# Kernel optimization log

Measured on AMD Instinct MI355X. Metric: run time of the kernel, lower is better.

Reference implementation:

```python
import jax, jax.numpy as jnp
import numpy as np
from jax import lax

B, C, H, W = 64, 512, 20, 15
N = H * W  # must be 300 (ChannelAttention dim)
EPS = 1e-5


def layernorm(x, w, b):
    m = x.mean(-1, keepdims=True)
    v = x.var(-1, keepdims=True)
    return (x - m) * lax.rsqrt(v + EPS) * w + b


def batchnorm(x, w, b):  # training-mode BN over (B,H,W), x: (B,C,H,W)
    m = x.mean((0, 2, 3), keepdims=True)
    v = x.var((0, 2, 3), keepdims=True)
    return (x - m) * lax.rsqrt(v + EPS) * w[None, :, None, None] + b[None, :, None, None]


def cross_linear_attn(x1, x2, kv1_w, kv2_w, heads):
    # x: (B, n, c); kv_w: (2c, c). Linear-attention variant: softmax over channel axis of k^T v.
    b, n, c = x1.shape
    d = c // heads
    scale = d ** -0.5

    def split_q(x):
        return x.reshape(b, n, heads, d).transpose(0, 2, 1, 3)  # (b,h,n,d)

    def kv(x, w):
        t = (x @ w.T).reshape(b, n, 2, heads, d).transpose(2, 0, 3, 1, 4)
        return t[0], t[1]  # each (b,h,n,d)

    q1, q2 = split_q(x1), split_q(x2)
    k1, v1 = kv(x1, kv1_w)
    k2, v2 = kv(x2, kv2_w)

    def ctx(k, v):  # (b,h,d,d), softmax over dim -2
        return jax.nn.softmax(jnp.einsum('bhnd,bhne->bhde', k, v) * scale, axis=-2)

    c1, c2 = ctx(k1, v1), ctx(k2, v2)

    def out(q, cx):
        return jnp.einsum('bhnd,bhde->bhne', q, cx).transpose(0, 2, 1, 3).reshape(b, n, c)

    return out(q1, c2), out(q2, c1)  # cross: q1 uses ctx2, q2 uses ctx1


def conv1x1(x, w):  # x: (B,Ci,H,W), w: (Co,Ci)
    return jnp.einsum('oi,bihw->bohw', w, x)


def setup_inputs() -> dict:
    key = jax.random.key(0)
    ks = jax.random.split(key, 24)
    g = lambda i, shape, s=0.02: jax.random.normal(ks[i], shape, jnp.float32) * s
    inp = {
        'x1': jax.random.normal(ks[0], (B, C, H, W), jnp.float32),
        'x2': jax.random.normal(ks[1], (B, C, H, W), jnp.float32),
        # CrossPath channel_proj1/2: Linear(C, 2C) + LayerNorm(2C)
        'cp1_w': g(2, (2 * C, C)), 'cp1_b': jnp.zeros((2 * C,), jnp.float32),
        'ln1_w': jnp.ones((2 * C,), jnp.float32), 'ln1_b': jnp.zeros((2 * C,), jnp.float32),
        'cp2_w': g(3, (2 * C, C)), 'cp2_b': jnp.zeros((2 * C,), jnp.float32),
        'ln2_w': jnp.ones((2 * C,), jnp.float32), 'ln2_b': jnp.zeros((2 * C,), jnp.float32),
        # SpatialAttention (dim=C, heads=8) kv linears, no bias
        's_kv1_w': g(4, (2 * C, C)), 's_kv2_w': g(5, (2 * C, C)),
        # ChannelAttention (dim=N=300, heads=4) kv linears, no bias
        'c_kv1_w': g(6, (2 * N, N)), 'c_kv2_w': g(7, (2 * N, N)),
        # ChannelEmbed(2C -> C)
        'res_w': g(8, (C, 2 * C), np.sqrt(2.0 / C)),
        'ce1_w': g(9, (C, 2 * C), np.sqrt(2.0 / C)), 'ce1_b': jnp.zeros((C,), jnp.float32),
        'dw_w': g(10, (C, 1, 3, 3), np.sqrt(2.0 / 9.0)), 'dw_b': jnp.zeros((C,), jnp.float32),
        'ce3_w': g(11, (C, C), np.sqrt(2.0 / C)), 'ce3_b': jnp.zeros((C,), jnp.float32),
        'bn_e_w': jnp.ones((C,), jnp.float32), 'bn_e_b': jnp.zeros((C,), jnp.float32),
        'bn_o_w': jnp.ones((C,), jnp.float32), 'bn_o_b': jnp.zeros((C,), jnp.float32),
    }
    return inp


def reference(x1, x2, cp1_w, cp1_b, ln1_w, ln1_b, cp2_w, cp2_b, ln2_w, ln2_b,
              s_kv1_w, s_kv2_w, c_kv1_w, c_kv2_w,
              res_w, ce1_w, ce1_b, dw_w, dw_b, ce3_w, ce3_b,
              bn_e_w, bn_e_b, bn_o_w, bn_o_b):
    b, c, h, w = x1.shape
    n = h * w
    t1 = x1.reshape(b, c, n).transpose(0, 2, 1)  # (B,N,C)
    t2 = x2.reshape(b, c, n).transpose(0, 2, 1)

    a1 = jax.nn.relu(layernorm(t1 @ cp1_w.T + cp1_b, ln1_w, ln1_b))
    a2 = jax.nn.relu(layernorm(t2 @ cp2_w.T + cp2_b, ln2_w, ln2_b))
    c1, s1 = a1[..., :c], a1[..., c:]
    c2, s2 = a2[..., :c], a2[..., c:]

    v1, v2 = cross_linear_attn(s1, s2, s_kv1_w, s_kv2_w, heads=8)
    z1, z2 = cross_linear_attn(c1.transpose(0, 2, 1), c2.transpose(0, 2, 1),
                               c_kv1_w, c_kv2_w, heads=4)
    s = v1 + v2                                  # (B,N,C)
    cc = (z1 + z2).transpose(0, 2, 1)            # (B,N,C)

    merge = jnp.concatenate([s, cc], axis=-1)    # (B,N,2C)
    xm = merge.transpose(0, 2, 1).reshape(b, 2 * c, h, w)

    residual = conv1x1(xm, res_w)
    e = conv1x1(xm, ce1_w) + ce1_b[None, :, None, None]
    e = lax.conv_general_dilated(e, dw_w, (1, 1), 'SAME',
                                 dimension_numbers=('NCHW', 'OIHW', 'NCHW'),
                                 feature_group_count=c) + dw_b[None, :, None, None]
    e = jnp.where(e >= 0, e, 0.01 * e)  # LeakyReLU(0.01)
    e = conv1x1(e, ce3_w) + ce3_b[None, :, None, None]
    e = batchnorm(e, bn_e_w, bn_e_b)
    return batchnorm(residual + e, bn_o_w, bn_o_b)
```

## Files before the change

### kernel.cpp

```cpp
#include <hip/hip_runtime.h>

typedef unsigned short u16;
typedef __attribute__((ext_vector_type(8))) short bh8;
typedef __attribute__((ext_vector_type(4))) float f4;

__device__ __forceinline__ u16 f2b(float f){
  unsigned int u = __float_as_uint(f);
  u += 0x7fffu + ((u >> 16) & 1u);
  return (u16)(u >> 16);
}
__device__ __forceinline__ float b2f(u16 h){
  return __uint_as_float(((unsigned int)h) << 16);
}
__device__ __forceinline__ void gl16(const u16* g, u16* l){
  __builtin_amdgcn_global_load_lds((const __attribute__((address_space(1))) void*)g,
                                   (__attribute__((address_space(3))) void*)l, 16, 0, 0);
}

__global__ void pack_plain(const float* __restrict__ src, u16* __restrict__ dst, int count){
  int i = blockIdx.x*256 + threadIdx.x;
  if (i < count) dst[i] = f2b(src[i]);
}
__global__ void pack_ckv_k(const float* __restrict__ src, u16* __restrict__ dst){
  int i = blockIdx.x*256 + threadIdx.x;
  int nn = i / 320, kk = i - (i/320)*320;
  int t_ = (nn >= 320) ? 1 : 0;
  int rem = nn - t_*320;
  int hh = rem / 80, dd = rem - hh*80;
  int kh = kk / 80, kd = kk - kh*80;
  float v = 0.f;
  if (dd < 75 && kd < 75)
    v = src[(size_t)(t_*300 + hh*75 + dd)*300 + (kh*75 + kd)];
  dst[i] = f2b(v);
}
__global__ void pack_dw(const float* __restrict__ src, u16* __restrict__ dst){
  int i = blockIdx.x*256 + threadIdx.x;
  if (i < 4608){
    int t = i >> 9, c = i & 511;
    dst[i] = f2b(src[c*9 + t]);
  }
}
__global__ void pad_zero(u16* __restrict__ slack){
  const int j = blockIdx.x*256 + threadIdx.x;
  if (j < 2048) slack[j] = 0;
}

__global__ __launch_bounds__(256)
void transpose_k(const float* __restrict__ x, u16* __restrict__ t)
{
  __shared__ float tile[32][33];
  const int n0 = blockIdx.x * 32, c0 = blockIdx.y * 32, b = blockIdx.z;
  const int ln = threadIdx.x & 31, lr = threadIdx.x >> 5;
  #pragma unroll
  for (int q = 0; q < 4; q++) {
    const int c = c0 + lr + q*8, n = n0 + ln;
    tile[lr + q*8][ln] = (n < 300) ? x[((long)b*512 + c)*300 + n] : 0.f;
  }
  __syncthreads();
  #pragma unroll
  for (int q = 0; q < 4; q++) {
    const int n = n0 + lr + q*8;
    if (n < 300) t[((long)b*300 + n)*512 + c0 + ln] = f2b(tile[ln][lr + q*8]);
  }
}

template<int OUTF, int HASB>
__global__ __launch_bounds__(512, 2)
void gemm256(const u16* __restrict__ A, int lda,
             const u16* __restrict__ Bw, const u16* __restrict__ Bw2, int ldb, long mhalf,
             u16* __restrict__ Cb, float* __restrict__ Cf, int ldc,
             const float* __restrict__ bias, const float* __restrict__ bias2, int K)
{
  __shared__ u16 As[2][16384];
  __shared__ u16 Bs[2][16384];
  const int tid = threadIdx.x;
  const int gx = gridDim.x;
  const int nwg = gx * gridDim.y;
  const int flat = blockIdx.y * gx + blockIdx.x;
  const int qq = nwg >> 3, rr = nwg & 7, xcd = flat & 7, lin = flat >> 3;
  const int newid = (xcd < rr ? xcd*(qq+1) : rr*(qq+1) + (xcd-rr)*qq) + lin;
  const long n0 = (long)(newid % gx) * 256;
  const long m0 = (long)(newid / gx) * 256;
  const u16* Bwp = Bw; const float* bp = bias;
  if (Bw2 != nullptr && m0 >= mhalf){ Bwp = Bw2; bp = bias2; }
  const int wave = tid >> 6, lane = tid & 63;
  const int l15 = lane & 15, lg = lane >> 4;
  const int wr = (wave >> 2) * 128;
  const int wc = (wave & 3) * 64;
  const int srow = tid >> 3;
  const int gseg = ((tid & 7) ^ (srow & 7)) * 8;
  const u16* Ag[4]; const u16* Bg[4];
  #pragma unroll
  for (int q = 0; q < 4; q++){
    Ag[q] = A   + (m0 + q*64 + srow) * (long)lda + gseg;
    Bg[q] = Bwp + (n0 + q*64 + srow) * (long)ldb + gseg;
  }
  int roA[8], roB[4];
  #pragma unroll
  for (int i = 0; i < 8; i++){ const int rA = wr + i*16 + l15; roA[i] = rA*64 + ((lg ^ (rA & 7)) * 8); }
  #pragma unroll
  for (int i = 0; i < 4; i++){ const int rB = wc + i*16 + l15; roB[i] = rB*64 + ((lg ^ (rB & 7)) * 8); }
  f4 acc[8][4] = {};
  const int NT = K >> 6;
  #pragma unroll
  for (int q = 0; q < 4; q++){
    gl16(Ag[q], &As[0][(q*512 + tid)*8]);
    gl16(Bg[q], &Bs[0][(q*512 + tid)*8]);
  }
  asm volatile("s_waitcnt vmcnt(0)" ::: "memory");
  __builtin_amdgcn_sched_barrier(0);
  __builtin_amdgcn_s_barrier();
  __builtin_amdgcn_sched_barrier(0);
  int cur = 0;
  for (int t = 0; t < NT; t++) {
    if (t + 1 < NT) {
      const int kt = (t + 1) << 6;
      const int nb = cur ^ 1;
      #pragma unroll
      for (int q = 0; q < 4; q++){
        gl16(Ag[q] + kt, &As[nb][(q*512 + tid)*8]);
        gl16(Bg[q] + kt, &Bs[nb][(q*512 + tid)*8]);
      }
    }
    #pragma unroll
    for (int ks = 0; ks < 2; ks++){
      const int kx = ks * 32;
      bh8 af[8], bf[4];
      #pragma unroll
      for (int mi = 0; mi < 8; mi++) af[mi] = *(const bh8*)&As[cur][roA[mi] ^ kx];
      #pragma unroll
      for (int ni = 0; ni < 4; ni++) bf[ni] = *(const bh8*)&Bs[cur][roB[ni] ^ kx];
      __builtin_amdgcn_s_setprio(1);
      #pragma unroll
      for (int mi = 0; mi < 8; mi++)
        #pragma unroll
        for (int ni = 0; ni < 4; ni++)
          acc[mi][ni] = __builtin_amdgcn_mfma_f32_16x16x32_bf16(af[mi], bf[ni], acc[mi][ni], 0, 0, 0);
      __builtin_amdgcn_s_setprio(0);
    }
    if (t + 1 < NT) {
      asm volatile("s_waitcnt vmcnt(0)" ::: "memory");
      __builtin_amdgcn_sched_barrier(0);
      __builtin_amdgcn_s_barrier();
      __builtin_amdgcn_sched_barrier(0);
      cur ^= 1;
    }
  }
  if (OUTF == 2) {
    u16* resb16 = (u16*)Cf;
    if (n0 < 512) {
      #pragma unroll
      for (int ni = 0; ni < 4; ni++) {
        const long cn = n0 + wc + ni*16 + l15;
        #pragma unroll
        for (int mi = 0; mi < 8; mi++)
          #pragma unroll
          for (int r = 0; r < 4; r++) {
            const long cm = m0 + wr + mi*16 + lg*4 + r;
            resb16[cm * ldc + cn] = f2b(acc[mi][ni][r]);
          }
      }
    } else {
      #pragma unroll
      for (int ni = 0; ni < 4; ni++) {
        const long cn = n0 - 512 + wc + ni*16 + l15;
        const float bv = bias[cn];
        #pragma unroll
        for (int mi = 0; mi < 8; mi++)
          #pragma unroll
          for (int r = 0; r < 4; r++) {
            const long cm = m0 + wr + mi*16 + lg*4 + r;
            Cb[cm * ldc + cn] = f2b(acc[mi][ni][r] + bv);
          }
      }
    }
  } else {
    #pragma unroll
    for (int ni = 0; ni < 4; ni++) {
      const long cn = n0 + wc + ni*16 + l15;
      const float bv = HASB ? bp[cn] : 0.0f;
      #pragma unroll
      for (int mi = 0; mi < 8; mi++)
        #pragma unroll
        for (int r = 0; r < 4; r++) {
          const long cm = m0 + wr + mi*16 + lg*4 + r;
          Cb[cm * ldc + cn] = f2b(acc[mi][ni][r] + bv);
        }
    }
  }
}

template<int OUTF, int HASB>
__global__ __launch_bounds__(512)
void gemm_k(const u16* __restrict__ A, int lda,
            const u16* __restrict__ Bw, const u16* __restrict__ Bw2, int ldb, long mhalf,
            u16* __restrict__ Cb, float* __restrict__ Cf, int ldc,
            const float* __restrict__ bias, const float* __restrict__ bias2, int K)
{
  __shared__ u16 As[3][8192];
  __shared__ u16 Bs[3][4096];
  const int tid = threadIdx.x;
  const int gx = gridDim.x;
  const int nwg = gx * gridDim.y;
  const int flat = blockIdx.y * gx + blockIdx.x;
  const int qq = nwg >> 3, rr = nwg & 7, xcd = flat & 7, lin = flat >> 3;
  const int newid = (xcd < rr ? xcd*(qq+1) : rr*(qq+1) + (xcd-rr)*qq) + lin;
  const long n0 = (long)(newid % gx) * 128;
  const long m0 = (long)(newid / gx) * 256;
  const u16* Bwp = Bw; const float* bp = bias;
  if (Bw2 != nullptr && m0 >= mhalf){ Bwp = Bw2; bp = bias2; }
  const int wave = tid >> 6, lane = tid & 63;
  const int l15 = lane & 15, lg = lane >> 4;
  const int wr = (wave >> 1) * 64, wc = (wave & 1) * 64;
  const int arow = tid >> 2;
  const int aseg = ((tid & 3) ^ ((arow >> 1) & 3)) * 8;
  const u16* Ag0 = A + (m0 + arow) * (long)lda + aseg;
  const u16* Ag1 = A + (m0 + 128 + arow) * (long)lda + aseg;
  const u16* Bg0 = Bwp + (n0 + arow) * (long)ldb + aseg;
  const int to8 = tid * 8;
  int roA[4], roB[4];
  #pragma unroll
  for (int i = 0; i < 4; i++){
    const int rA = wr + i*16 + l15;
    roA[i] = rA*32 + ((lg ^ ((rA >> 1) & 3)) * 8);
    const int rB = wc + i*16 + l15;
    roB[i] = rB*32 + ((lg ^ ((rB >> 1) & 3)) * 8);
  }
  f4 acc[4][4] = {};
  const int NT = K >> 5;
  {
    gl16(Ag0, &As[0][to8]); gl16(Ag1, &As[0][4096 + to8]); gl16(Bg0, &Bs[0][to8]);
    gl16(Ag0 + 32, &As[1][to8]); gl16(Ag1 + 32, &As[1][4096 + to8]); gl16(Bg0 + 32, &Bs[1][to8]);
  }
  int rd = 0;
  for (int t = 0; t < NT; t++) {
    if (t < NT - 1) { asm volatile("s_waitcnt vmcnt(3)" ::: "memory"); }
    else            { asm volatile("s_waitcnt vmcnt(0)" ::: "memory"); }
    __builtin_amdgcn_sched_barrier(0);
    __builtin_amdgcn_s_barrier();
    __builtin_amdgcn_sched_barrier(0);
    if (t + 2 < NT) {
      int wb = rd + 2; if (wb >= 3) wb -= 3;
      const int kt = (t + 2) << 5;
      gl16(Ag0 + kt, &As[wb][to8]); gl16(Ag1 + kt, &As[wb][4096 + to8]); gl16(Bg0 + kt, &Bs[wb][to8]);
    }
    bh8 af[4], bf[4];
    #pragma unroll
    for (int mi = 0; mi < 4; mi++) af[mi] = *(const bh8*)&As[rd][roA[mi]];
    #pragma unroll
    for (int ni = 0; ni < 4; ni++) bf[ni] = *(const bh8*)&Bs[rd][roB[ni]];
    #pragma unroll
    for (int mi = 0; mi < 4; mi++)
      #pragma unroll
      for (int ni = 0; ni < 4; ni++)
        acc[mi][ni] = __builtin_amdgcn_mfma_f32_16x16x32_bf16(af[mi], bf[ni], acc[mi][ni], 0, 0, 0);
    rd++; if (rd == 3) rd = 0;
  }
  #pragma unroll
  for (int ni = 0; ni < 4; ni++) {
    const long cn = n0 + wc + ni*16 + l15;
    const float bv = HASB ? bp[cn] : 0.0f;
    #pragma unroll
    for (int mi = 0; mi < 4; mi++) {
      #pragma unroll
      for (int r = 0; r < 4; r++) {
        const long cm = m0 + wr + mi*16 + lg*4 + r;
        const float v = acc[mi][ni][r] + bv;
        if (OUTF) Cf[cm * ldc + cn] = v;
        else      Cb[cm * ldc + cn] = f2b(v);
      }
    }
  }
}

__global__ __launch_bounds__(256)
void ln_kernel(const u16* __restrict__ apre, const float* __restrict__ lw, const float* __restrict__ lb,
               u16* __restrict__ s, u16* __restrict__ cT)
{
  __shared__ u16 tile[40][520];
  const int bh = blockIdx.x;
  const int b = bh >> 2, h = bh & 3;
  const int z = blockIdx.y;
  const int dd0 = z ? 40 : 0;
  const int ndd = z ? 35 : 40;
  const int segbase = z ? 5 : 0;
  const int tid = threadIdx.x, w = tid >> 6, lane = tid & 63;
  const int r0 = b*300 + h*75 + dd0;
  for (int dl = w; dl < ndd; dl += 4){
    const int r = r0 + dl;
    const u16* row = apre + (size_t)r*1024 + lane*8;
    const bh8 vc = *(const bh8*)row;
    const bh8 vs = *(const bh8*)(row + 512);
    float fc[8], fs[8];
    float sm = 0.f, sq = 0.f;
    #pragma unroll
    for (int j = 0; j < 8; j++){
      fc[j] = b2f((u16)vc[j]); fs[j] = b2f((u16)vs[j]);
      sm += fc[j] + fs[j];
      sq += fc[j]*fc[j] + fs[j]*fs[j];
    }
    #pragma unroll
    for (int o = 32; o; o >>= 1){ sm += __shfl_xor(sm, o); sq += __shfl_xor(sq, o); }
    const float mean = sm * (1.f/1024.f);
    const float rstd = rsqrtf(sq*(1.f/1024.f) - mean*mean + 1e-5f);
    bh8 oc, os;
    #pragma unroll
    for (int j = 0; j < 8; j++){
      const int c = lane*8 + j;
      const float y1 = (fc[j]-mean)*rstd*lw[c] + lb[c];
      oc[j] = (short)f2b(fmaxf(y1, 0.f));
      const float y2 = (fs[j]-mean)*rstd*lw[512+c] + lb[512+c];
      os[j] = (short)f2b(fmaxf(y2, 0.f));
    }
    *(bh8*)&tile[dl][lane*8] = oc;
    *(bh8*)&s[(size_t)r*512 + lane*8] = os;
  }
  __syncthreads();
  for (int i = tid; i < 2560; i += 256){
    const int c = i / 5, sg = i - (i/5)*5;
    const int seg = segbase + sg;
    bh8 ov;
    #pragma unroll
    for (int j = 0; j < 8; j++){
      const int dl = seg*8 + j - dd0;
      ov[j] = (short)((dl >= 0 && dl < ndd) ? tile[dl][c] : (u16)0);
    }
    *(bh8*)&cT[((size_t)b*512 + c)*320 + h*80 + seg*8] = ov;
  }
}

template<int D, int DREAL, int OS>
__global__ __launch_bounds__(256)
void ctx_kernel(const u16* __restrict__ kva, const u16* __restrict__ kvb,
                u16* __restrict__ outp, int K, int RS, int VOFF, float scale)
{
  constexpr int NT = D/16, MT = D/16, MTL = (MT+3)/4, SEG = D/8;
  __shared__ u16 vT[D][40];
  __shared__ u16 kT[D][40];
  const int h = blockIdx.x, b = blockIdx.y, iq = blockIdx.z;
  const int Hn = gridDim.x;
  const u16* base = (iq ? kvb : kva) + (size_t)b*K*RS + h*D;
  u16* out = outp + (((size_t)iq*64 + b)*Hn + h)*(size_t)(D*OS);
  const int tid = threadIdx.x, w = tid >> 6, lane = tid & 63, l15 = lane & 15, lg = lane >> 4;
  f4 acc[MTL][NT] = {};
  for (int k0 = 0; k0 < K; k0 += 32) {
    __syncthreads();
    for (int sI = tid; sI < 32*SEG; sI += 256) {
      const int nn = sI / SEG, dseg = sI - (sI/SEG)*SEG;
      bh8 kk = {}, vv = {};
      const int krow = k0 + nn;
      if (krow < K) {
        const u16* p = base + (size_t)krow*RS + dseg*8;
        kk = *(const bh8*)p;
        vv = *(const bh8*)(p + VOFF);
      }
      #pragma unroll
      for (int j = 0; j < 8; j++){
        kT[dseg*8+j][nn] = (u16)kk[j];
        vT[dseg*8+j][nn] = (u16)vv[j];
      }
    }
    __syncthreads();
    #pragma unroll
    for (int ii = 0; ii < MTL; ii++){
      const int mt = w + ii*4;
      if (MT % 4 != 0 && mt >= MT) break;
      const bh8 a = *(const bh8*)&vT[mt*16 + l15][lg*8];
      #pragma unroll
      for (int nt = 0; nt < NT; nt++){
        const bh8 bb = *(const bh8*)&kT[nt*16 + l15][lg*8];
        acc[ii][nt] = __builtin_amdgcn_mfma_f32_16x16x32_bf16(a, bb, acc[ii][nt], 0, 0, 0);
      }
    }
  }
  #pragma unroll
  for (int ii = 0; ii < MTL; ii++){
    const int mt = w + ii*4;
    if (MT % 4 != 0 && mt >= MT) continue;
    #pragma unroll
    for (int r = 0; r < 4; r++){
      const int e = mt*16 + lg*4 + r;
      float xs[NT]; float mx = -1e30f;
      #pragma unroll
      for (int nt = 0; nt < NT; nt++){
        float x = acc[ii][nt][r] * scale;
        if (DREAL != D && (nt*16 + l15) >= DREAL) x = -1e30f;
        xs[nt] = x; mx = fmaxf(mx, x);
      }
      mx = fmaxf(mx, __shfl_xor(mx,1)); mx = fmaxf(mx, __shfl_xor(mx,2));
      mx = fmaxf(mx, __shfl_xor(mx,4)); mx = fmaxf(mx, __shfl_xor(mx,8));
      float smv = 0.f;
      #pragma unroll
      for (int nt = 0; nt < NT; nt++){
        const float p = (xs[nt] > -1e29f) ? __expf(xs[nt]-mx) : 0.f;
        xs[nt] = p; smv += p;
      }
      smv += __shfl_xor(smv,1); smv += __shfl_xor(smv,2);
      smv += __shfl_xor(smv,4); smv += __shfl_xor(smv,8);
      const float inv = 1.f / smv;
      #pragma unroll
      for (int nt = 0; nt < NT; nt++)
        out[(size_t)e*OS + nt*16 + l15] = f2b(xs[nt]*inv);
      if (OS > D) out[(size_t)e*OS + D + l15] = 0;
    }
  }
}

__global__ __launch_bounds__(256)
void sp_out_kernel(const u16* __restrict__ s1, const u16* __restrict__ s2,
                   const u16* __restrict__ csT, u16* __restrict__ merge)
{
  const int h = blockIdx.x, b = blockIdx.y;
  const int tid = threadIdx.x, w = tid >> 6, lane = tid & 63, l15 = lane & 15, lg = lane >> 4;
  const u16* c1 = csT + (((size_t)b)*8 + h)*4096;
  const u16* c2 = csT + (((size_t)64 + b)*8 + h)*4096;
  for (int mt = w; mt < 19; mt += 4) {
    const int m = mt*16 + l15;
    const bool mv = (m < 300);
    const u16* q1 = s1 + ((size_t)b*300 + m)*512 + h*64;
    const u16* q2 = s2 + ((size_t)b*300 + m)*512 + h*64;
    f4 acc[4] = {};
    #pragma unroll
    for (int kc = 0; kc < 2; kc++){
      bh8 a1 = {}, a2 = {};
      if (mv){ a1 = *(const bh8*)(q1 + kc*32 + lg*8); a2 = *(const bh8*)(q2 + kc*32 + lg*8); }
      #pragma unroll
      for (int nt = 0; nt < 4; nt++){
        const bh8 b2v = *(const bh8*)&c2[(size_t)(nt*16+l15)*64 + kc*32 + lg*8];
        acc[nt] = __builtin_amdgcn_mfma_f32_16x16x32_bf16(a1, b2v, acc[nt], 0, 0, 0);
        const bh8 b1v = *(const bh8*)&c1[(size_t)(nt*16+l15)*64 + kc*32 + lg*8];
        acc[nt] = __builtin_amdgcn_mfma_f32_16x16x32_bf16(a2, b1v, acc[nt], 0, 0, 0);
      }
    }
    #pragma unroll
    for (int nt = 0; nt < 4; nt++)
      #pragma unroll
      for (int r = 0; r < 4; r++){
        const int mm = mt*16 + lg*4 + r;
        if (mm < 300)
          merge[((size_t)b*300 + mm)*1024 + h*64 + nt*16 + l15] = f2b(acc[nt][r]);
      }
  }
}

__global__ __launch_bounds__(256)
void ch_out_kernel(const u16* __restrict__ cT1, const u16* __restrict__ cT2,
                   const u16* __restrict__ ccT, u16* __restrict__ merge)
{
  const int cb = blockIdx.x, h = blockIdx.y, b = blockIdx.z;
  const int tid = threadIdx.x, w = tid >> 6, lane = tid & 63, l15 = lane & 15, lg = lane >> 4;
  const int chbase = cb*128 + w*32;
  f4 acc[5][2] = {};
  #pragma unroll
  for (int oi = 0; oi < 2; oi++){
    const u16* Am = ccT + (((size_t)((oi==0)?1:0)*64 + b)*4 + h)*(size_t)(80*96);
    const u16* qb = (oi==0) ? cT1 : cT2;
    #pragma unroll
    for (int kc = 0; kc < 3; kc++){
      bh8 bf[2];
      #pragma unroll
      for (int nf = 0; nf < 2; nf++){
        const int ch = chbase + nf*16 + l15;
        bf[nf] = *(const bh8*)&qb[((size_t)b*512 + ch)*320 + h*80 + kc*32 + lg*8];
      }
      #pragma unroll
      for (int mt = 0; mt < 5; mt++){
        const bh8 a = *(const bh8*)&Am[(size_t)(mt*16+l15)*96 + kc*32 + lg*8];
        #pragma unroll
        for (int nf = 0; nf < 2; nf++)
          acc[mt][nf] = __builtin_amdgcn_mfma_f32_16x16x32_bf16(a, bf[nf], acc[mt][nf], 0, 0, 0);
      }
    }
  }
  #pragma unroll
  for (int mt = 0; mt < 5; mt++)
    #pragma unroll
    for (int nf = 0; nf < 2; nf++)
      #pragma unroll
      for (int r = 0; r < 4; r++){
        const int e = mt*16 + lg*4 + r;
        if (e < 75)
          merge[((size_t)b*300 + h*75 + e)*1024 + 512 + chbase + nf*16 + l15] = f2b(acc[mt][nf][r]);
      }
}

__global__ __launch_bounds__(256)
void dw_kernel(const u16* __restrict__ e1, const u16* __restrict__ dwt,
               const float* __restrict__ bias, u16* __restrict__ d1)
{
  const int idx = blockIdx.x*256 + threadIdx.x;
  const int cg = idx & 63;
  const int sp = (idx >> 6) % 300;
  const int b  = idx / (64*300);
  const int c0 = cg*8;
  const int hh = sp / 15, ww = sp - hh*15;
  float acc[8];
  {
    const float4 b0 = *(const float4*)&bias[c0];
    const float4 b1 = *(const float4*)&bias[c0+4];
    acc[0]=b0.x; acc[1]=b0.y; acc[2]=b0.z; acc[3]=b0.w;
    acc[4]=b1.x; acc[5]=b1.y; acc[6]=b1.z; acc[7]=b1.w;
  }
  #pragma unroll
  for (int dy = -1; dy <= 1; dy++){
    const int h2 = hh + dy; if (h2 < 0 || h2 >= 20) continue;
    #pragma unroll
    for (int dx = -1; dx <= 1; dx++){
      const int w2 = ww + dx; if (w2 < 0 || w2 >= 15) continue;
      const bh8 vv = *(const bh8*)&e1[((size_t)b*300 + h2*15 + w2)*512 + c0];
      const int t = (dy+1)*3 + (dx+1);
      const bh8 wv = *(const bh8*)&dwt[t*512 + c0];
      #pragma unroll
      for (int j = 0; j < 8; j++)
        acc[j] += b2f((u16)vv[j]) * b2f((u16)wv[j]);
    }
  }
  bh8 ov;
  #pragma unroll
  for (int j = 0; j < 8; j++){
    float y = acc[j];
    y = (y >= 0.f) ? y : 0.01f*y;
    ov[j] = (short)f2b(y);
  }
  *(bh8*)&d1[((size_t)b*300 + sp)*512 + c0] = ov;
}

__global__ __launch_bounds__(256)
void stats_k(const u16* __restrict__ e3, const u16* __restrict__ res, float* __restrict__ st){
  const int tid = threadIdx.x;
  const int c0 = tid*2;
  const size_t r0 = (size_t)blockIdx.x * 128;
  float se0=0,se1=0,qe0=0,qe1=0,sr0=0,sr1=0,qr0=0,qr1=0,x0=0,x1=0;
  for (int rr = 0; rr < 128; rr++){
    const size_t o2 = (r0+rr)*512 + c0;
    const unsigned int eu = *(const unsigned int*)&e3[o2];
    const unsigned int ru = *(const unsigned int*)&res[o2];
    const float ex = b2f((u16)(eu & 0xffff)), ey = b2f((u16)(eu >> 16));
    const float rx = b2f((u16)(ru & 0xffff)), ry = b2f((u16)(ru >> 16));
    se0 += ex; se1 += ey; qe0 += ex*ex; qe1 += ey*ey;
    sr0 += rx; sr1 += ry; qr0 += rx*rx; qr1 += ry*ry;
    x0  += ex*rx; x1 += ey*ry;
  }
  atomicAdd(&st[c0], se0);      atomicAdd(&st[c0+1], se1);
  atomicAdd(&st[512+c0], qe0);  atomicAdd(&st[512+c0+1], qe1);
  atomicAdd(&st[1024+c0], sr0); atomicAdd(&st[1024+c0+1], sr1);
  atomicAdd(&st[1536+c0], qr0); atomicAdd(&st[1536+c0+1], qr1);
  atomicAdd(&st[2048+c0], x0);  atomicAdd(&st[2048+c0+1], x1);
}
__global__ void fin_k(float* st, const float* __restrict__ we, const float* __restrict__ be,
                      const float* __restrict__ wo, const float* __restrict__ bo){
  const int c = threadIdx.x;
  const float Nf = 19200.f, iN = 1.f/19200.f;
  const float Se = st[c], Qe = st[512+c], Sr = st[1024+c], Qr = st[1536+c], X = st[2048+c];
  const float me = Se*iN;
  const float ve = Qe*iN - me*me;
  const float ae = we[c]*rsqrtf(ve + 1e-5f);
  const float bev = be[c] - me*ae;
  const float So = Sr + ae*Se + Nf*bev;
  const float Qo = Qr + ae*ae*Qe + Nf*bev*bev + 2.f*ae*X + 2.f*bev*Sr + 2.f*ae*bev*Se;
  const float mo = So*iN;
  const float vo = Qo*iN - mo*mo;
  const float ao = wo[c]*rsqrtf(vo + 1e-5f);
  const float bov = bo[c] - mo*ao;
  st[2560+c] = ae; st[3072+c] = bev; st[3584+c] = ao; st[4096+c] = bov;
}
__global__ __launch_bounds__(256)
void final_kernel(const u16* __restrict__ res, const u16* __restrict__ e3,
                  const float* __restrict__ st, float* __restrict__ outp)
{
  __shared__ float tile[64][65];
  const int spt = blockIdx.x, cht = blockIdx.y, b = blockIdx.z;
  const int tid = threadIdx.x;
  const int sp0 = spt*64, ch0 = cht*64;
  for (int idx = tid; idx < 2048; idx += 256){
    const int cl = (idx & 31)*2, sl = idx >> 5;
    const int sp = sp0 + sl;
    float v0 = 0.f, v1 = 0.f;
    if (sp < 300){
      const size_t off = ((size_t)b*300 + sp)*512 + ch0 + cl;
      const int c = ch0 + cl;
      const unsigned int eu = *(const unsigned int*)&e3[off];
      const unsigned int ru = *(const unsigned int*)&res[off];
      const float e0 = b2f((u16)(eu & 0xffff))*st[2560+c]   + st[3072+c];
      const float e1 = b2f((u16)(eu >> 16))   *st[2560+c+1] + st[3072+c+1];
      v0 = (b2f((u16)(ru & 0xffff)) + e0)*st[3584+c]   + st[4096+c];
      v1 = (b2f((u16)(ru >> 16))    + e1)*st[3584+c+1] + st[4096+c+1];
    }
    tile[sl][cl] = v0; tile[sl][cl+1] = v1;
  }
  __syncthreads();
  for (int idx = tid; idx < 4096; idx += 256){
    const int sl = idx & 63, cl = idx >> 6;
    const int sp = sp0 + sl;
    if (sp < 300)
      outp[((size_t)b*512 + ch0 + cl)*300 + sp] = tile[sl][cl];
  }
}

extern "C" void kernel_launch(void* const* d_in, const int* in_sizes, int n_in,
                              void* d_out, int out_size, void* d_ws, size_t ws_size,
                              hipStream_t stream)
{
  const float* x1    = (const float*)d_in[0];
  const float* x2    = (const float*)d_in[1];
  const float* cp1_w = (const float*)d_in[2];
  const float* cp1_b = (const float*)d_in[3];
  const float* ln1_w = (const float*)d_in[4];
  const float* ln1_b = (const float*)d_in[5];
  const float* cp2_w = (const float*)d_in[6];
  const float* cp2_b = (const float*)d_in[7];
  const float* ln2_w = (const float*)d_in[8];
  const float* ln2_b = (const float*)d_in[9];
  const float* skv1w = (const float*)d_in[10];
  const float* skv2w = (const float*)d_in[11];
  const float* ckv1w = (const float*)d_in[12];
  const float* ckv2w = (const float*)d_in[13];
  const float* resw  = (const float*)d_in[14];
  const float* ce1w  = (const float*)d_in[15];
  const float* ce1b  = (const float*)d_in[16];
  const float* dww   = (const float*)d_in[17];
  const float* dwb   = (const float*)d_in[18];
  const float* ce3w  = (const float*)d_in[19];
  const float* ce3b  = (const float*)d_in[20];
  const float* bnew  = (const float*)d_in[21];
  const float* bneb  = (const float*)d_in[22];
  const float* bnow  = (const float*)d_in[23];
  const float* bnob  = (const float*)d_in[24];
  float* out = (float*)d_out;
  char* ws = (char*)d_ws;

  const size_t SZ_T    = (size_t)19200*512*2;
  const size_t SZ_APRE = (size_t)19200*1024*2;
  const size_t SZ_CKV  = (size_t)32768*640*2;
  const size_t SZ_CT   = (size_t)64*512*320*2;
  const size_t SZ_F32  = (size_t)19200*512*4;

  size_t off = 0;
  auto AL = [&](size_t sz){ size_t r = off; off += (sz + 255) & ~(size_t)255; return r; };
  const size_t oR0 = AL(2*SZ_T);
  const size_t oR1 = AL(2*SZ_CKV);
  const size_t oR2 = AL(2*SZ_T);
  const size_t oR3 = AL(2*SZ_CT + 4096);
  const size_t oR4 = AL(SZ_F32);
  const size_t oR5 = AL((size_t)2*64*8*64*64*2);
  const size_t oR6 = AL((size_t)2*64*4*80*96*2);
  const size_t oWcp1  = AL((size_t)1024*512*2);
  const size_t oWcp2  = AL((size_t)1024*512*2);
  const size_t oWskv1 = AL((size_t)1024*512*2);
  const size_t oWskv2 = AL((size_t)1024*512*2);
  const size_t oWckv1 = AL((size_t)640*320*2);
  const size_t oWckv2 = AL((size_t)640*320*2);
  const size_t oWresce = AL((size_t)1024*1024*2);
  const size_t oWce3  = AL((size_t)512*512*2);
  const size_t oWdw   = AL((size_t)9*512*2);
  const size_t oST    = AL(20480);
  (void)ws_size; (void)in_sizes; (void)n_in; (void)out_size;

  u16* t1    = (u16*)(ws + oR0);
  u16* merge = (u16*)(ws + oR0);
  u16* apre1 = (u16*)(ws + oR1);
  u16* ckv1  = (u16*)(ws + oR1);
  u16* s1    = (u16*)(ws + oR2);
  u16* s2    = (u16*)(ws + oR2 + SZ_T);
  u16* e1    = s1;
  u16* d1    = s2;
  u16* cT1   = (u16*)(ws + oR3);
  u16* cT2   = (u16*)(ws + oR3 + SZ_CT);
  u16* slack = (u16*)(ws + oR3 + 2*SZ_CT);
  u16* e3b   = (u16*)(ws + oR3);
  u16* resb  = (u16*)(ws + oR4);
  u16* csT   = (u16*)(ws + oR5);
  u16* ccT   = (u16*)(ws + oR6);
  u16* wcp1  = (u16*)(ws + oWcp1);
  u16* wcp2  = (u16*)(ws + oWcp2);
  u16* wskv1 = (u16*)(ws + oWskv1);
  u16* wskv2 = (u16*)(ws + oWskv2);
  u16* wckv1 = (u16*)(ws + oWckv1);
  u16* wckv2 = (u16*)(ws + oWckv2);
  u16* wresce = (u16*)(ws + oWresce);
  u16* wce3  = (u16*)(ws + oWce3);
  u16* wdw   = (u16*)(ws + oWdw);
  float* st  = (float*)(ws + oST);

  u16* t2    = t1 + 19200*512;
  u16* kv1   = apre1;
  u16* ckv2  = ckv1 + (size_t)32768*640;

  hipMemsetAsync(st, 0, 10240, stream);
  pad_zero<<<8,256,0,stream>>>(slack);
  pack_plain<<<2048,256,0,stream>>>(cp1_w, wcp1, 524288);
  pack_plain<<<2048,256,0,stream>>>(cp2_w, wcp2, 524288);
  pack_plain<<<2048,256,0,stream>>>(skv1w, wskv1, 524288);
  pack_plain<<<2048,256,0,stream>>>(skv2w, wskv2, 524288);
  pack_ckv_k<<<800,256,0,stream>>>(ckv1w, wckv1);
  pack_ckv_k<<<800,256,0,stream>>>(ckv2w, wckv2);
  pack_plain<<<2048,256,0,stream>>>(resw, wresce, 524288);
  pack_plain<<<2048,256,0,stream>>>(ce1w, wresce + 524288, 524288);
  pack_plain<<<1024,256,0,stream>>>(ce3w, wce3, 262144);
  pack_dw<<<18,256,0,stream>>>(dww, wdw);

  transpose_k<<<dim3(10,16,64),256,0,stream>>>(x1, t1);
  transpose_k<<<dim3(10,16,64),256,0,stream>>>(x2, t2);

  gemm256<0,1><<<dim3(4,150),512,0,stream>>>(t1,512, wcp1,wcp2,512, 19200L,
                                             apre1,nullptr,1024, cp1_b,cp2_b, 512);

  ln_kernel<<<dim3(256,2),256,0,stream>>>(apre1, ln1_w, ln1_b, s1, cT1);
  ln_kernel<<<dim3(256,2),256,0,stream>>>(apre1 + (size_t)19200*1024, ln2_w, ln2_b, s2, cT2);

  gemm256<0,0><<<dim3(4,150),512,0,stream>>>(s1,512, wskv1,wskv2,512, 19200L,
                                             kv1,nullptr,1024, nullptr,nullptr, 512);

  ctx_kernel<64,64,64><<<dim3(8,64,2),256,0,stream>>>(kv1, kv1 + (size_t)19200*1024, csT, 300, 1024, 512, 0.125f);

  gemm_k<0,0><<<dim3(5,256),512,0,stream>>>(cT1,320, wckv1,wckv2,320, 32768L,
                                            ckv1,nullptr,640, nullptr,nullptr, 320);

  ctx_kernel<80,75,96><<<dim3(4,64,2),256,0,stream>>>(ckv1, ckv2, ccT, 512, 640, 320, 0.115470054f);

  sp_out_kernel<<<dim3(8,64),256,0,stream>>>(s1, s2, csT, merge);
  ch_out_kernel<<<dim3(4,4,64),256,0,stream>>>(cT1, cT2, ccT, merge);

  gemm256<2,0><<<dim3(4,75),512,0,stream>>>(merge,1024, wresce,nullptr,1024, (long)1<<40,
                                            e1, (float*)resb, 512, ce1b,nullptr, 1024);

  dw_kernel<<<4800,256,0,stream>>>(e1, wdw, dwb, d1);

  gemm_k<0,1><<<dim3(4,75),512,0,stream>>>(d1,512, wce3,nullptr,512, (long)1<<40,
                                           e3b,nullptr,512, ce3b,nullptr, 512);

  stats_k<<<150,256,0,stream>>>(e3b, resb, st);
  fin_k<<<1,512,0,stream>>>(st, bnew, bneb, bnow, bnob);
  final_kernel<<<dim3(5,8,64),256,0,stream>>>(resb, e3b, st, out);
}
```

Before: 558.3 us.

## Halve GEMM K-tile to 32 with two-stage prefetch and higher occupancy

```diff
diff --git a/kernel.cpp b/kernel.cpp
--- a/kernel.cpp
+++ b/kernel.cpp
@@ -65,14 +65,14 @@
 }
 
 template<int OUTF, int HASB>
-__global__ __launch_bounds__(512, 2)
-void gemm256(const u16* __restrict__ A, int lda,
-             const u16* __restrict__ Bw, const u16* __restrict__ Bw2, int ldb, long mhalf,
-             u16* __restrict__ Cb, float* __restrict__ Cf, int ldc,
-             const float* __restrict__ bias, const float* __restrict__ bias2, int K)
-{
-  __shared__ u16 As[2][16384];
-  __shared__ u16 Bs[2][16384];
+__global__ __launch_bounds__(512, 4)
+void gemm2(const u16* __restrict__ A, int lda,
+           const u16* __restrict__ Bw, const u16* __restrict__ Bw2, int ldb, long mhalf,
+           u16* __restrict__ Cb, float* __restrict__ Cf, int ldc,
+           const float* __restrict__ bias, const float* __restrict__ bias2, int K)
+{
+  __shared__ u16 As[2][8192];
+  __shared__ u16 Bs[2][8192];
   const int tid = threadIdx.x;
   const int gx = gridDim.x;
   const int nwg = gx * gridDim.y;
@@ -87,63 +87,57 @@
   const int l15 = lane & 15, lg = lane >> 4;
   const int wr = (wave >> 2) * 128;
   const int wc = (wave & 3) * 64;
-  const int srow = tid >> 3;
-  const int gseg = ((tid & 7) ^ (srow & 7)) * 8;
-  const u16* Ag[4]; const u16* Bg[4];
-  #pragma unroll
-  for (int q = 0; q < 4; q++){
-    Ag[q] = A   + (m0 + q*64 + srow) * (long)lda + gseg;
-    Bg[q] = Bwp + (n0 + q*64 + srow) * (long)ldb + gseg;
-  }
+  const int srow = tid >> 2;
+  const int gseg = ((tid & 3) ^ ((tid >> 3) & 3)) * 8;
+  const u16* Ag0 = A   + (m0 + srow)       * (long)lda + gseg;
+  const u16* Ag1 = A   + (m0 + 128 + srow) * (long)lda + gseg;
+  const u16* Bg0 = Bwp + (n0 + srow)       * (long)ldb + gseg;
+  const u16* Bg1 = Bwp + (n0 + 128 + srow) * (long)ldb + gseg;
+  const int to8 = tid * 8;
   int roA[8], roB[4];
   #pragma unroll
-  for (int i = 0; i < 8; i++){ const int rA = wr + i*16 + l15; roA[i] = rA*64 + ((lg ^ (rA & 7)) * 8); }
-  #pragma unroll
-  for (int i = 0; i < 4; i++){ const int rB = wc + i*16 + l15; roB[i] = rB*64 + ((lg ^ (rB & 7)) * 8); }
+  for (int i = 0; i < 8; i++){ const int rA = wr + i*16 + l15; roA[i] = rA*32 + ((lg ^ ((rA >> 1) & 3)) * 8); }
+  #pragma unroll
+  for (int i = 0; i < 4; i++){ const int rB = wc + i*16 + l15; roB[i] = rB*32 + ((lg ^ ((rB >> 1) & 3)) * 8); }
   f4 acc[8][4] = {};
-  const int NT = K >> 6;
-  #pragma unroll
-  for (int q = 0; q < 4; q++){
-    gl16(Ag[q], &As[0][(q*512 + tid)*8]);
-    gl16(Bg[q], &Bs[0][(q*512 + tid)*8]);
-  }
-  asm volatile("s_waitcnt vmcnt(0)" ::: "memory");
+  const int NT = K >> 5;
+  gl16(Ag0,      &As[0][to8]); gl16(Ag1,      &As[0][4096 + to8]);
+  gl16(Bg0,      &Bs[0][to8]); gl16(Bg1,      &Bs[0][4096 + to8]);
+  gl16(Ag0 + 32, &As[1][to8]); gl16(Ag1 + 32, &As[1][4096 + to8]);
+  gl16(Bg0 + 32, &Bs[1][to8]); gl16(Bg1 + 32, &Bs[1][4096 + to8]);
+  asm volatile("s_waitcnt vmcnt(4)" ::: "memory");
   __builtin_amdgcn_sched_barrier(0);
   __builtin_amdgcn_s_barrier();
   __builtin_amdgcn_sched_barrier(0);
-  int cur = 0;
   for (int t = 0; t < NT; t++) {
+    const int cur = t & 1;
+    bh8 af[8], bf[4];
+    #pragma unroll
+    for (int mi = 0; mi < 8; mi++) af[mi] = *(const bh8*)&As[cur][roA[mi]];
+    #pragma unroll
+    for (int ni = 0; ni < 4; ni++) bf[ni] = *(const bh8*)&Bs[cur][roB[ni]];
+    __builtin_amdgcn_s_setprio(1);
+    #pragma unroll
+    for (int mi = 0; mi < 8; mi++)
+      #pragma unroll
+      for (int ni = 0; ni < 4; ni++)
+        acc[mi][ni] = __builtin_amdgcn_mfma_f32_16x16x32_bf16(af[mi], bf[ni], acc[mi][ni], 0, 0, 0);
+    __builtin_amdgcn_s_setprio(0);
     if (t + 1 < NT) {
-      const int kt = (t + 1) << 6;
-      const int nb = cur ^ 1;
-      #pragma unroll
-      for (int q = 0; q < 4; q++){
-        gl16(Ag[q] + kt, &As[nb][(q*512 + tid)*8]);
-        gl16(Bg[q] + kt, &Bs[nb][(q*512 + tid)*8]);
-      }
-    }
-    #pragma unroll
-    for (int ks = 0; ks < 2; ks++){
-      const int kx = ks * 32;
-      bh8 af[8], bf[4];
-      #pragma unroll
-      for (int mi = 0; mi < 8; mi++) af[mi] = *(const bh8*)&As[cur][roA[mi] ^ kx];
-      #pragma unroll
-      for (int ni = 0; ni < 4; ni++) bf[ni] = *(const bh8*)&Bs[cur][roB[ni] ^ kx];
-      __builtin_amdgcn_s_setprio(1);
-      #pragma unroll
-      for (int mi = 0; mi < 8; mi++)
-        #pragma unroll
-        for (int ni = 0; ni < 4; ni++)
-          acc[mi][ni] = __builtin_amdgcn_mfma_f32_16x16x32_bf16(af[mi], bf[ni], acc[mi][ni], 0, 0, 0);
-      __builtin_amdgcn_s_setprio(0);
-    }
-    if (t + 1 < NT) {
-      asm volatile("s_waitcnt vmcnt(0)" ::: "memory");
       __builtin_amdgcn_sched_barrier(0);
       __builtin_amdgcn_s_barrier();
       __builtin_amdgcn_sched_barrier(0);
-      cur ^= 1;
+      if (t + 2 < NT) {
+        const int kt = (t + 2) << 5;
+        gl16(Ag0 + kt, &As[cur][to8]); gl16(Ag1 + kt, &As[cur][4096 + to8]);
+        gl16(Bg0 + kt, &Bs[cur][to8]); gl16(Bg1 + kt, &Bs[cur][4096 + to8]);
+        asm volatile("s_waitcnt vmcnt(4)" ::: "memory");
+      } else {
+        asm volatile("s_waitcnt vmcnt(0)" ::: "memory");
+      }
+      __builtin_amdgcn_sched_barrier(0);
+      __builtin_amdgcn_s_barrier();
+      __builtin_amdgcn_sched_barrier(0);
     }
   }
   if (OUTF == 2) {
@@ -702,14 +696,14 @@
   transpose_k<<<dim3(10,16,64),256,0,stream>>>(x1, t1);
   transpose_k<<<dim3(10,16,64),256,0,stream>>>(x2, t2);
 
-  gemm256<0,1><<<dim3(4,150),512,0,stream>>>(t1,512, wcp1,wcp2,512, 19200L,
-                                             apre1,nullptr,1024, cp1_b,cp2_b, 512);
+  gemm2<0,1><<<dim3(4,150),512,0,stream>>>(t1,512, wcp1,wcp2,512, 19200L,
+                                           apre1,nullptr,1024, cp1_b,cp2_b, 512);
 
   ln_kernel<<<dim3(256,2),256,0,stream>>>(apre1, ln1_w, ln1_b, s1, cT1);
   ln_kernel<<<dim3(256,2),256,0,stream>>>(apre1 + (size_t)19200*1024, ln2_w, ln2_b, s2, cT2);
 
-  gemm256<0,0><<<dim3(4,150),512,0,stream>>>(s1,512, wskv1,wskv2,512, 19200L,
-                                             kv1,nullptr,1024, nullptr,nullptr, 512);
+  gemm2<0,0><<<dim3(4,150),512,0,stream>>>(s1,512, wskv1,wskv2,512, 19200L,
+                                           kv1,nullptr,1024, nullptr,nullptr, 512);
 
   ctx_kernel<64,64,64><<<dim3(8,64,2),256,0,stream>>>(kv1, kv1 + (size_t)19200*1024, csT, 300, 1024, 512, 0.125f);
 
@@ -721,13 +715,13 @@
   sp_out_kernel<<<dim3(8,64),256,0,stream>>>(s1, s2, csT, merge);
   ch_out_kernel<<<dim3(4,4,64),256,0,stream>>>(cT1, cT2, ccT, merge);
 
-  gemm256<2,0><<<dim3(4,75),512,0,stream>>>(merge,1024, wresce,nullptr,1024, (long)1<<40,
-                                            e1, (float*)resb, 512, ce1b,nullptr, 1024);
+  gemm2<2,0><<<dim3(4,75),512,0,stream>>>(merge,1024, wresce,nullptr,1024, (long)1<<40,
+                                          e1, (float*)resb, 512, ce1b,nullptr, 1024);
 
   dw_kernel<<<4800,256,0,stream>>>(e1, wdw, dwb, d1);
 
-  gemm_k<0,1><<<dim3(4,75),512,0,stream>>>(d1,512, wce3,nullptr,512, (long)1<<40,
-                                           e3b,nullptr,512, ce3b,nullptr, 512);
+  gemm2<0,1><<<dim3(2,75),512,0,stream>>>(d1,512, wce3,nullptr,512, (long)1<<40,
+                                          e3b,nullptr,512, ce3b,nullptr, 512);
 
   stats_k<<<150,256,0,stream>>>(e3b, resb, st);
   fin_k<<<1,512,0,stream>>>(st, bnew, bneb, bnow, bnob);
```

Result: slower. 2.025 ms (+262.7%).
